# Kernel optimization log

Measured on AMD Instinct MI355X. Metric: run time of the kernel, lower is better.

## Reference

```python
import jax, jax.numpy as jnp
import numpy as np
import math

B, T = 64, 2000
RNN_DIM, EMB_DIM, ATT_DIM = 1024, 512, 128
STATIC_CH, STATIC_K = 8, 21
DYN_CH, DYN_K = 8, 21
PRIOR_LEN, ALPHA, BETA = 11, 0.1, 0.9


def _betabinom_pmf(k, n, a, b):
    lg = math.lgamma
    return math.exp(lg(n + 1) - lg(k + 1) - lg(n - k + 1)
                    + lg(k + a) + lg(n - k + b) - lg(n + a + b)
                    - (lg(a) + lg(b) - lg(a + b)))


def setup_inputs() -> dict:
    key = jax.random.key(0)
    ks = jax.random.split(key, 12)
    query = jax.random.normal(ks[0], (B, RNN_DIM), jnp.float32)
    memory = jax.random.normal(ks[1], (B, T, EMB_DIM), jnp.float32)
    a = jax.random.uniform(ks[2], (B, T), jnp.float32)
    alignment_pre = a / jnp.sum(a, axis=1, keepdims=True)  # valid attention distribution
    mask = jnp.zeros((B, T), dtype=bool)
    s = 1.0 / math.sqrt(RNN_DIM)
    W_w = jax.random.uniform(ks[3], (ATT_DIM, RNN_DIM), jnp.float32, -s, s)
    W_b = jax.random.uniform(ks[4], (ATT_DIM,), jnp.float32, -s, s)
    V_w = jax.random.normal(ks[5], (DYN_CH * DYN_K, ATT_DIM), jnp.float32) * 0.05
    F_w = jax.random.normal(ks[6], (STATIC_CH, 1, STATIC_K), jnp.float32) * 0.1
    U_w = jax.random.normal(ks[7], (ATT_DIM, STATIC_CH), jnp.float32) * 0.1
    T_w = jax.random.normal(ks[8], (ATT_DIM, DYN_CH), jnp.float32) * 0.1
    T_b = jax.random.normal(ks[9], (ATT_DIM,), jnp.float32) * 0.05
    v_w = jax.random.normal(ks[10], (1, ATT_DIM), jnp.float32) * 0.1
    P_np = np.array([_betabinom_pmf(k, PRIOR_LEN - 1, ALPHA, BETA) for k in range(PRIOR_LEN)], np.float32)
    P = jnp.asarray(P_np[::-1].copy())  # buffer: flipped beta-binomial prior
    return {"attention_hidden_state": query, "memory": memory, "alignment_pre": alignment_pre,
            "mask": mask, "W_w": W_w, "W_b": W_b, "V_w": V_w, "F_w": F_w,
            "U_w": U_w, "T_w": T_w, "T_b": T_b, "v_w": v_w, "P": P}


def _conv1d(lhs, rhs, pad, groups=1):
    # lhs [N,C,T], rhs [O,C//groups,K]; cross-correlation, matching torch conv1d
    return jax.lax.conv_general_dilated(lhs, rhs, (1,), [pad],
                                        dimension_numbers=("NCH", "OIH", "NCH"),
                                        feature_group_count=groups)


def reference(attention_hidden_state, memory, alignment_pre, mask,
              W_w, W_b, V_w, F_w, U_w, T_w, T_b, v_w, P):
    b, t = alignment_pre.shape
    # log of causal beta-binomial prior: left-pad by prior_length-1, valid conv
    p = _conv1d(alignment_pre[:, None, :], P.reshape(1, 1, -1), (PRIOR_LEN - 1, 0))[:, 0, :]
    p = jnp.log(jnp.clip(p, 1e-6))
    # per-sample dynamic kernels: [B, dyn_ch*K]
    G = jnp.tanh(attention_hidden_state @ W_w.T + W_b) @ V_w.T
    g = _conv1d(alignment_pre[None, :, :], G.reshape(b * DYN_CH, 1, DYN_K),
                ((DYN_K - 1) // 2, (DYN_K - 1) // 2), groups=b)  # [1, B*dyn_ch, T]
    g = g.reshape(b, DYN_CH, t).transpose(0, 2, 1)  # [B, T, dyn_ch]
    # static conv features
    f = _conv1d(alignment_pre[:, None, :], F_w,
                ((STATIC_K - 1) // 2, (STATIC_K - 1) // 2)).transpose(0, 2, 1)  # [B, T, static_ch]
    e = (jnp.tanh(f @ U_w.T + g @ T_w.T + T_b) @ v_w.T)[..., 0] + p  # [B, T]
    e = jnp.where(mask, -jnp.inf, e)
    attention_weights = jax.nn.softmax(e, axis=1)
    attention_context = jnp.einsum("bt,bte->be", attention_weights, memory)
    return attention_context, attention_weights
```

## Files before the change

### kernel.cpp

```cpp
#include <hip/hip_runtime.h>

#define B_   64
#define T_   2000
#define RNN_ 1024
#define EMB_ 512
#define ATT_ 128
#define CH_  8
#define K_   21
#define PL_  11
#define GSZ  168
#define ECHK 128
#define NEC  16
#define NCS  16
#define CPS  32
#define WSEG 125

typedef float vf4 __attribute__((ext_vector_type(4)));

__device__ __forceinline__ float fast_tanh(float x) {
    float ax = fabsf(x);
    float e  = __expf(2.0f * ax);
    float t  = 1.0f - 2.0f / (e + 1.0f);
    return copysignf(t, x);
}

__global__ __launch_bounds__(256) void k_gen_dyn(
    const float* __restrict__ q, const float* __restrict__ Ww,
    const float* __restrict__ Wb, const float* __restrict__ Vw,
    float* __restrict__ G)
{
    __shared__ float sq[RNN_];
    __shared__ float part[256];
    __shared__ float sh[ATT_];
    const int b = blockIdx.x, tid = threadIdx.x;
    for (int i = tid; i < RNN_; i += 256) sq[i] = q[b * RNN_ + i];
    __syncthreads();
    {
        const int row = tid & 127, half = tid >> 7;
        const float4* wr = reinterpret_cast<const float4*>(Ww + row * RNN_ + half * (RNN_ / 2));
        const float4* qr = reinterpret_cast<const float4*>(sq + half * (RNN_ / 2));
        float acc = 0.f;
        #pragma unroll 8
        for (int i = 0; i < RNN_ / 8; ++i) {
            float4 w4 = wr[i], q4 = qr[i];
            acc += w4.x * q4.x + w4.y * q4.y + w4.z * q4.z + w4.w * q4.w;
        }
        part[tid] = acc;
    }
    __syncthreads();
    if (tid < ATT_) sh[tid] = fast_tanh(part[tid] + part[tid + 128] + Wb[tid]);
    __syncthreads();
    for (int o = tid; o < GSZ; o += 256) {
        const float4* vr = reinterpret_cast<const float4*>(Vw + o * ATT_);
        const float4* hr = reinterpret_cast<const float4*>(sh);
        float acc = 0.f;
        #pragma unroll 8
        for (int i = 0; i < ATT_ / 4; ++i) {
            float4 v4 = vr[i], h4 = hr[i];
            acc += v4.x * h4.x + v4.y * h4.y + v4.z * h4.z + v4.w * h4.w;
        }
        G[b * GSZ + o] = acc;
    }
}

__global__ __launch_bounds__(256) void k_energy(
    const float* __restrict__ a,  const float* __restrict__ G,
    const float* __restrict__ Fw, const float* __restrict__ Uw,
    const float* __restrict__ Tw, const float* __restrict__ Tb,
    const float* __restrict__ vw, const float* __restrict__ P,
    const unsigned char* __restrict__ mask,
    float* __restrict__ pws, float* __restrict__ mred, float* __restrict__ sred)
{
    __shared__ float sA[ECHK + K_ - 1];
    __shared__ float sFG[K_ * 16];
    __shared__ float sUT[ATT_ * 16];
    __shared__ float sTb[ATT_], sV[ATT_], sPr[PL_];
    __shared__ float sQ[2 * ECHK];
    __shared__ float red[4];
    const int b = blockIdx.x, chunk = blockIdx.y, tid = threadIdx.x;
    const int t0 = chunk * ECHK;
    const int base = t0 - (K_ - 1) / 2;
    const int tloc = tid & (ECHK - 1);
    const int h = tid >> 7;

    for (int j = tid; j < ECHK + K_ - 1; j += 256) {
        int idx = base + j;
        sA[j] = (idx >= 0 && idx < T_) ? a[b * T_ + idx] : 0.f;
    }
    for (int j = tid; j < 2 * GSZ; j += 256) {
        if (j < GSZ) sFG[(j % K_) * 16 + (j / K_)] = Fw[j];
        else { int jj = j - GSZ; sFG[(jj % K_) * 16 + 8 + (jj / K_)] = G[b * GSZ + jj]; }
    }
    for (int j = tid; j < ATT_ * CH_; j += 256) {
        int d = j >> 3, c = j & 7;
        sUT[d * 16 + c]     = Uw[j];
        sUT[d * 16 + 8 + c] = Tw[j];
    }
    if (tid < ATT_) { sTb[tid] = Tb[tid]; sV[tid] = vw[tid]; }
    if (tid < PL_)  sPr[tid] = P[tid];
    __syncthreads();

    float fg[16];
    #pragma unroll
    for (int i = 0; i < 16; ++i) fg[i] = 0.f;
    #pragma unroll
    for (int k = 0; k < K_; ++k) {
        float av = sA[tloc + k];
        const float4* fp = reinterpret_cast<const float4*>(&sFG[k * 16]);
        float4 x0 = fp[0], x1 = fp[1], x2 = fp[2], x3 = fp[3];
        fg[0]  += x0.x * av; fg[1]  += x0.y * av; fg[2]  += x0.z * av; fg[3]  += x0.w * av;
        fg[4]  += x1.x * av; fg[5]  += x1.y * av; fg[6]  += x1.z * av; fg[7]  += x1.w * av;
        fg[8]  += x2.x * av; fg[9]  += x2.y * av; fg[10] += x2.z * av; fg[11] += x2.w * av;
        fg[12] += x3.x * av; fg[13] += x3.y * av; fg[14] += x3.z * av; fg[15] += x3.w * av;
    }

    float accQ = 0.f;
    const int d0 = h * 64;
    #pragma unroll 4
    for (int dd = 0; dd < 64; ++dd) {
        const int d = d0 + dd;
        const float4* up = reinterpret_cast<const float4*>(&sUT[d * 16]);
        float4 u0 = up[0], u1 = up[1], u2 = up[2], u3 = up[3];
        float s0 = u0.x * fg[0]  + u0.y * fg[1]  + u0.z * fg[2]  + u0.w * fg[3];
        float s1 = u1.x * fg[4]  + u1.y * fg[5]  + u1.z * fg[6]  + u1.w * fg[7];
        float s2 = u2.x * fg[8]  + u2.y * fg[9]  + u2.z * fg[10] + u2.w * fg[11];
        float s3 = u3.x * fg[12] + u3.y * fg[13] + u3.z * fg[14] + u3.w * fg[15];
        float s = (sTb[d] + s0) + (s1 + s2) + s3;
        accQ += sV[d] * fast_tanh(s);
    }
    sQ[h * ECHK + tloc] = accQ;
    __syncthreads();

    float e = -1e30f;
    const int t = t0 + tid;
    if (tid < ECHK) {
        const bool valid = (t < T_) && !mask[b * T_ + min(t, T_ - 1)];
        if (valid) {
            float pp = 0.f;
            #pragma unroll
            for (int k = 0; k < PL_; ++k) pp += sPr[k] * sA[tid + k];
            e = sQ[tid] + sQ[ECHK + tid] + __logf(fmaxf(pp, 1e-6f));
        }
    }
    float m = e;
    #pragma unroll
    for (int off = 32; off > 0; off >>= 1) m = fmaxf(m, __shfl_xor(m, off));
    if ((tid & 63) == 0) red[tid >> 6] = m;
    __syncthreads();
    const float Mc = fmaxf(fmaxf(red[0], red[1]), fmaxf(red[2], red[3]));
    __syncthreads();
    float pv = (e > -1e29f) ? __expf(e - Mc) : 0.f;
    if (tid < ECHK && t < T_) pws[b * T_ + t] = pv;
    float ssum = pv;
    #pragma unroll
    for (int off = 32; off > 0; off >>= 1) ssum += __shfl_xor(ssum, off);
    if ((tid & 63) == 0) red[tid >> 6] = ssum;
    __syncthreads();
    if (tid == 0) {
        mred[b * NEC + chunk] = Mc;
        sred[b * NEC + chunk] = red[0] + red[1] + red[2] + red[3];
    }
}

__global__ __launch_bounds__(256) void k_ctx(
    const float* __restrict__ mred, const float* __restrict__ sred,
    const float* __restrict__ pws, const float* __restrict__ mem,
    float* __restrict__ wout, float* __restrict__ out)
{
    __shared__ float sAl[NEC];
    __shared__ float sw_[T_];
    __shared__ vf4 sPart[32][8];
    const int b = blockIdx.x, cs = blockIdx.y, tid = threadIdx.x;

    if (tid < NEC) {
        float M = -1e30f;
        #pragma unroll
        for (int i = 0; i < NEC; ++i) M = fmaxf(M, mred[b * NEC + i]);
        float S = 0.f;
        #pragma unroll
        for (int i = 0; i < NEC; ++i) S += sred[b * NEC + i] * __expf(mred[b * NEC + i] - M);
        sAl[tid] = __expf(mred[b * NEC + tid] - M) / S;
    }
    __syncthreads();
    for (int j = tid; j < T_; j += 256) sw_[j] = pws[b * T_ + j] * sAl[j >> 7];
    __syncthreads();
    if (tid < WSEG) {
        const int t = cs * WSEG + tid;
        wout[b * T_ + t] = sw_[t];
    }

    const int lane = tid & 7, rgrp = tid >> 3;
    const float* basep = mem + (size_t)b * T_ * EMB_ + cs * CPS + lane * 4;
    vf4 acc = {0.f, 0.f, 0.f, 0.f};
    #pragma unroll 8
    for (int i = 0; i < 62; ++i) {
        const int t = rgrp + i * 32;
        vf4 mv = *reinterpret_cast<const vf4*>(basep + (size_t)t * EMB_);
        acc += sw_[t] * mv;
    }
    if (rgrp < 16) {
        const int t = rgrp + 1984;
        vf4 mv = *reinterpret_cast<const vf4*>(basep + (size_t)t * EMB_);
        acc += sw_[t] * mv;
    }
    sPart[rgrp][lane] = acc;
    __syncthreads();
    if (tid < 64) {
        const int l = tid & 7, qg = tid >> 3;
        vf4 r = sPart[qg][l] + sPart[qg + 8][l] + sPart[qg + 16][l] + sPart[qg + 24][l];
        sPart[qg][l] = r;
    }
    __syncthreads();
    if (tid < 8) {
        vf4 r = sPart[0][tid] + sPart[1][tid] + sPart[2][tid] + sPart[3][tid]
              + sPart[4][tid] + sPart[5][tid] + sPart[6][tid] + sPart[7][tid];
        *reinterpret_cast<vf4*>(out + b * EMB_ + cs * CPS + tid * 4) = r;
    }
}

extern "C" void kernel_launch(void* const* d_in, const int* in_sizes, int n_in,
                              void* d_out, int out_size, void* d_ws, size_t ws_size,
                              hipStream_t stream)
{
    const float* q    = (const float*)d_in[0];
    const float* mem  = (const float*)d_in[1];
    const float* a    = (const float*)d_in[2];
    const unsigned char* mask = (const unsigned char*)d_in[3];
    const float* Ww = (const float*)d_in[4];
    const float* Wb = (const float*)d_in[5];
    const float* Vw = (const float*)d_in[6];
    const float* Fw = (const float*)d_in[7];
    const float* Uw = (const float*)d_in[8];
    const float* Tw = (const float*)d_in[9];
    const float* Tb = (const float*)d_in[10];
    const float* vw = (const float*)d_in[11];
    const float* P  = (const float*)d_in[12];

    float* out_ctx = (float*)d_out;
    float* out_w   = out_ctx + B_ * EMB_;

    float* G    = (float*)d_ws;
    float* mred = G + B_ * GSZ;
    float* sred = mred + B_ * NEC;
    float* pws  = sred + B_ * NEC;

    k_gen_dyn<<<B_, 256, 0, stream>>>(q, Ww, Wb, Vw, G);
    k_energy<<<dim3(B_, NEC), 256, 0, stream>>>(a, G, Fw, Uw, Tw, Tb, vw, P,
                                                mask, pws, mred, sred);
    k_ctx<<<dim3(B_, NCS), 256, 0, stream>>>(mred, sred, pws, mem, out_w, out_ctx);
}
```

Before: 97.60 us.

## Fuse all three stages into one persistent kernel with per-batch grid barriers

Replaces the three kernel launches with a single 16x64-block kernel. The 16 blocks of each batch row cooperate through spin-wait barriers on global counters, first computing the hidden projection and the dynamic filters in split form, then energies for 125-step chunks. Each block then weights its own memory rows and atomically adds the partial context, which removes the pws round-trip and the launch gaps. The cost is a memset per call, spin-barrier latency, atomic contention on the output, and a deadlock risk if not all 1024 blocks can be resident at once.

After: 312.9 us. +220.6%, slower.

```diff
diff --git a/kernel.cpp b/kernel.cpp
--- a/kernel.cpp
+++ b/kernel.cpp
@@ -1,19 +1,16 @@
 #include <hip/hip_runtime.h>
 
-#define B_   64
-#define T_   2000
-#define RNN_ 1024
-#define EMB_ 512
-#define ATT_ 128
-#define CH_  8
-#define K_   21
-#define PL_  11
-#define GSZ  168
-#define ECHK 128
-#define NEC  16
-#define NCS  16
-#define CPS  32
-#define WSEG 125
+#define B_    64
+#define T_    2000
+#define RNN_  1024
+#define EMB_  512
+#define ATT_  128
+#define CH_   8
+#define K_    21
+#define PL_   11
+#define GSZ   168
+#define NC    16
+#define CROWS 125
 
 typedef float vf4 __attribute__((ext_vector_type(4)));
 
@@ -24,197 +21,224 @@
     return copysignf(t, x);
 }
 
-__global__ __launch_bounds__(256) void k_gen_dyn(
-    const float* __restrict__ q, const float* __restrict__ Ww,
-    const float* __restrict__ Wb, const float* __restrict__ Vw,
-    float* __restrict__ G)
+__device__ __forceinline__ void batch_bar(unsigned* bar, int slot, int b) {
+    __syncthreads();
+    if (threadIdx.x == 0) {
+        __threadfence();
+        unsigned* p = bar + slot * 64 + b;
+        atomicAdd(p, 1u);
+        long long tries = 0;
+        while (atomicAdd(p, 0u) < 16u) {
+            __builtin_amdgcn_s_sleep(2);
+            if (++tries > 200000000ll) break;
+        }
+        __threadfence();
+    }
+    __syncthreads();
+}
+
+__global__ __launch_bounds__(256, 4) void k_all(
+    const float* __restrict__ q,   const float* __restrict__ mem,
+    const float* __restrict__ a,   const unsigned char* __restrict__ mask,
+    const float* __restrict__ Ww,  const float* __restrict__ Wb,
+    const float* __restrict__ Vw,  const float* __restrict__ Fw,
+    const float* __restrict__ Uw,  const float* __restrict__ Tw,
+    const float* __restrict__ Tb,  const float* __restrict__ vw,
+    const float* __restrict__ P,
+    unsigned* __restrict__ bar,    float* __restrict__ h_ws,
+    float* __restrict__ G_ws,      float* __restrict__ mred,
+    float* __restrict__ sred,
+    float* __restrict__ out_ctx,   float* __restrict__ out_w)
 {
-    __shared__ float sq[RNN_];
-    __shared__ float part[256];
-    __shared__ float sh[ATT_];
-    const int b = blockIdx.x, tid = threadIdx.x;
-    for (int i = tid; i < RNN_; i += 256) sq[i] = q[b * RNN_ + i];
-    __syncthreads();
-    {
-        const int row = tid & 127, half = tid >> 7;
-        const float4* wr = reinterpret_cast<const float4*>(Ww + row * RNN_ + half * (RNN_ / 2));
-        const float4* qr = reinterpret_cast<const float4*>(sq + half * (RNN_ / 2));
+    __shared__ union {
+        struct { float q[RNN_]; float part[8][33]; } A;
+        struct { float h[ATT_]; float part[16][17]; } A2;
+        struct { float win[160]; float FG[K_ * 16]; float UT[ATT_ * 16];
+                 float Tb[ATT_]; float V[ATT_]; float Pr[12]; float Q[256];
+                 float red[4]; } B;
+        struct { float ms[32]; vf4 part[2][128]; } C;
+    } sm;
+    __shared__ float sp[128];
+
+    const int c = blockIdx.x, b = blockIdx.y, tid = threadIdx.x;
+    const int t0 = c * CROWS;
+
+    if (c == 0) {
+        for (int i = tid; i < EMB_; i += 256) out_ctx[b * EMB_ + i] = 0.f;
+    }
+    for (int i = tid; i < RNN_ / 4; i += 256)
+        reinterpret_cast<vf4*>(sm.A.q)[i] =
+            reinterpret_cast<const vf4*>(q + b * RNN_)[i];
+    __syncthreads();
+    {
+        const int dl = tid >> 5, ks = tid & 31;
+        const int d  = c * 8 + dl;
+        const vf4* wr = reinterpret_cast<const vf4*>(Ww + d * RNN_ + ks * 32);
+        const vf4* qr = reinterpret_cast<const vf4*>(sm.A.q + ks * 32);
         float acc = 0.f;
-        #pragma unroll 8
-        for (int i = 0; i < RNN_ / 8; ++i) {
-            float4 w4 = wr[i], q4 = qr[i];
+        #pragma unroll
+        for (int i = 0; i < 8; ++i) {
+            vf4 w4 = wr[i], q4 = qr[i];
             acc += w4.x * q4.x + w4.y * q4.y + w4.z * q4.z + w4.w * q4.w;
         }
-        part[tid] = acc;
-    }
-    __syncthreads();
-    if (tid < ATT_) sh[tid] = fast_tanh(part[tid] + part[tid + 128] + Wb[tid]);
-    __syncthreads();
-    for (int o = tid; o < GSZ; o += 256) {
-        const float4* vr = reinterpret_cast<const float4*>(Vw + o * ATT_);
-        const float4* hr = reinterpret_cast<const float4*>(sh);
+        sm.A.part[dl][ks] = acc;
+    }
+    __syncthreads();
+    if (tid < 8) {
+        float s = 0.f;
+        #pragma unroll
+        for (int i = 0; i < 32; ++i) s += sm.A.part[tid][i];
+        const int d = c * 8 + tid;
+        h_ws[b * ATT_ + d] = fast_tanh(s + Wb[d]);
+    }
+    batch_bar(bar, 0, b);
+
+    if (tid < ATT_) sm.A2.h[tid] = h_ws[b * ATT_ + tid];
+    __syncthreads();
+    {
+        const int j = tid >> 4, ks = tid & 15;
+        const int o = c * 11 + j;
         float acc = 0.f;
-        #pragma unroll 8
-        for (int i = 0; i < ATT_ / 4; ++i) {
-            float4 v4 = vr[i], h4 = hr[i];
-            acc += v4.x * h4.x + v4.y * h4.y + v4.z * h4.z + v4.w * h4.w;
-        }
-        G[b * GSZ + o] = acc;
-    }
-}
-
-__global__ __launch_bounds__(256) void k_energy(
-    const float* __restrict__ a,  const float* __restrict__ G,
-    const float* __restrict__ Fw, const float* __restrict__ Uw,
-    const float* __restrict__ Tw, const float* __restrict__ Tb,
-    const float* __restrict__ vw, const float* __restrict__ P,
-    const unsigned char* __restrict__ mask,
-    float* __restrict__ pws, float* __restrict__ mred, float* __restrict__ sred)
-{
-    __shared__ float sA[ECHK + K_ - 1];
-    __shared__ float sFG[K_ * 16];
-    __shared__ float sUT[ATT_ * 16];
-    __shared__ float sTb[ATT_], sV[ATT_], sPr[PL_];
-    __shared__ float sQ[2 * ECHK];
-    __shared__ float red[4];
-    const int b = blockIdx.x, chunk = blockIdx.y, tid = threadIdx.x;
-    const int t0 = chunk * ECHK;
-    const int base = t0 - (K_ - 1) / 2;
-    const int tloc = tid & (ECHK - 1);
-    const int h = tid >> 7;
-
-    for (int j = tid; j < ECHK + K_ - 1; j += 256) {
-        int idx = base + j;
-        sA[j] = (idx >= 0 && idx < T_) ? a[b * T_ + idx] : 0.f;
+        if (j < 11 && o < GSZ) {
+            const vf4* vr = reinterpret_cast<const vf4*>(Vw + o * ATT_ + ks * 8);
+            const vf4* hr = reinterpret_cast<const vf4*>(sm.A2.h + ks * 8);
+            vf4 v0 = vr[0], h0 = hr[0], v1 = vr[1], h1 = hr[1];
+            acc = v0.x * h0.x + v0.y * h0.y + v0.z * h0.z + v0.w * h0.w
+                + v1.x * h1.x + v1.y * h1.y + v1.z * h1.z + v1.w * h1.w;
+        }
+        sm.A2.part[j][ks] = acc;
+    }
+    __syncthreads();
+    if (tid < 11) {
+        const int o = c * 11 + tid;
+        if (o < GSZ) {
+            float s = 0.f;
+            #pragma unroll
+            for (int i = 0; i < 16; ++i) s += sm.A2.part[tid][i];
+            G_ws[b * GSZ + o] = s;
+        }
+    }
+    batch_bar(bar, 1, b);
+
+    for (int j = tid; j < CROWS + K_ - 1; j += 256) {
+        int idx = t0 - 10 + j;
+        sm.B.win[j] = (idx >= 0 && idx < T_) ? a[b * T_ + idx] : 0.f;
     }
     for (int j = tid; j < 2 * GSZ; j += 256) {
-        if (j < GSZ) sFG[(j % K_) * 16 + (j / K_)] = Fw[j];
-        else { int jj = j - GSZ; sFG[(jj % K_) * 16 + 8 + (jj / K_)] = G[b * GSZ + jj]; }
+        if (j < GSZ) sm.B.FG[(j % K_) * 16 + (j / K_)] = Fw[j];
+        else { int jj = j - GSZ; sm.B.FG[(jj % K_) * 16 + 8 + (jj / K_)] = G_ws[b * GSZ + jj]; }
     }
     for (int j = tid; j < ATT_ * CH_; j += 256) {
-        int d = j >> 3, c = j & 7;
-        sUT[d * 16 + c]     = Uw[j];
-        sUT[d * 16 + 8 + c] = Tw[j];
-    }
-    if (tid < ATT_) { sTb[tid] = Tb[tid]; sV[tid] = vw[tid]; }
-    if (tid < PL_)  sPr[tid] = P[tid];
-    __syncthreads();
-
-    float fg[16];
-    #pragma unroll
-    for (int i = 0; i < 16; ++i) fg[i] = 0.f;
-    #pragma unroll
-    for (int k = 0; k < K_; ++k) {
-        float av = sA[tloc + k];
-        const float4* fp = reinterpret_cast<const float4*>(&sFG[k * 16]);
-        float4 x0 = fp[0], x1 = fp[1], x2 = fp[2], x3 = fp[3];
-        fg[0]  += x0.x * av; fg[1]  += x0.y * av; fg[2]  += x0.z * av; fg[3]  += x0.w * av;
-        fg[4]  += x1.x * av; fg[5]  += x1.y * av; fg[6]  += x1.z * av; fg[7]  += x1.w * av;
-        fg[8]  += x2.x * av; fg[9]  += x2.y * av; fg[10] += x2.z * av; fg[11] += x2.w * av;
-        fg[12] += x3.x * av; fg[13] += x3.y * av; fg[14] += x3.z * av; fg[15] += x3.w * av;
-    }
-
-    float accQ = 0.f;
-    const int d0 = h * 64;
-    #pragma unroll 4
-    for (int dd = 0; dd < 64; ++dd) {
-        const int d = d0 + dd;
-        const float4* up = reinterpret_cast<const float4*>(&sUT[d * 16]);
-        float4 u0 = up[0], u1 = up[1], u2 = up[2], u3 = up[3];
-        float s0 = u0.x * fg[0]  + u0.y * fg[1]  + u0.z * fg[2]  + u0.w * fg[3];
-        float s1 = u1.x * fg[4]  + u1.y * fg[5]  + u1.z * fg[6]  + u1.w * fg[7];
-        float s2 = u2.x * fg[8]  + u2.y * fg[9]  + u2.z * fg[10] + u2.w * fg[11];
-        float s3 = u3.x * fg[12] + u3.y * fg[13] + u3.z * fg[14] + u3.w * fg[15];
-        float s = (sTb[d] + s0) + (s1 + s2) + s3;
-        accQ += sV[d] * fast_tanh(s);
-    }
-    sQ[h * ECHK + tloc] = accQ;
+        int d = j >> 3, ch = j & 7;
+        sm.B.UT[d * 16 + ch]     = Uw[j];
+        sm.B.UT[d * 16 + 8 + ch] = Tw[j];
+    }
+    if (tid < ATT_) { sm.B.Tb[tid] = Tb[tid]; sm.B.V[tid] = vw[tid]; }
+    if (tid < PL_)  sm.B.Pr[tid] = P[tid];
+    __syncthreads();
+
+    const int tloc = tid & 127, half = tid >> 7;
+    {
+        float fg[16];
+        #pragma unroll
+        for (int i = 0; i < 16; ++i) fg[i] = 0.f;
+        #pragma unroll
+        for (int k = 0; k < K_; ++k) {
+            float av = sm.B.win[tloc + k];
+            const vf4* fp = reinterpret_cast<const vf4*>(&sm.B.FG[k * 16]);
+            vf4 x0 = fp[0], x1 = fp[1], x2 = fp[2], x3 = fp[3];
+            fg[0]  += x0.x * av; fg[1]  += x0.y * av; fg[2]  += x0.z * av; fg[3]  += x0.w * av;
+            fg[4]  += x1.x * av; fg[5]  += x1.y * av; fg[6]  += x1.z * av; fg[7]  += x1.w * av;
+            fg[8]  += x2.x * av; fg[9]  += x2.y * av; fg[10] += x2.z * av; fg[11] += x2.w * av;
+            fg[12] += x3.x * av; fg[13] += x3.y * av; fg[14] += x3.z * av; fg[15] += x3.w * av;
+        }
+        float accQ = 0.f;
+        const int d0 = half * 64;
+        #pragma unroll 4
+        for (int dd = 0; dd < 64; ++dd) {
+            const int d = d0 + dd;
+            const vf4* up = reinterpret_cast<const vf4*>(&sm.B.UT[d * 16]);
+            vf4 u0 = up[0], u1 = up[1], u2 = up[2], u3 = up[3];
+            float s0 = u0.x * fg[0]  + u0.y * fg[1]  + u0.z * fg[2]  + u0.w * fg[3];
+            float s1 = u1.x * fg[4]  + u1.y * fg[5]  + u1.z * fg[6]  + u1.w * fg[7];
+            float s2 = u2.x * fg[8]  + u2.y * fg[9]  + u2.z * fg[10] + u2.w * fg[11];
+            float s3 = u3.x * fg[12] + u3.y * fg[13] + u3.z * fg[14] + u3.w * fg[15];
+            float s = (sm.B.Tb[d] + s0) + (s1 + s2) + s3;
+            accQ += sm.B.V[d] * fast_tanh(s);
+        }
+        sm.B.Q[half * 128 + tloc] = accQ;
+    }
     __syncthreads();
 
     float e = -1e30f;
-    const int t = t0 + tid;
-    if (tid < ECHK) {
-        const bool valid = (t < T_) && !mask[b * T_ + min(t, T_ - 1)];
-        if (valid) {
+    if (tid < CROWS) {
+        const int t = t0 + tid;
+        if (!mask[b * T_ + t]) {
             float pp = 0.f;
             #pragma unroll
-            for (int k = 0; k < PL_; ++k) pp += sPr[k] * sA[tid + k];
-            e = sQ[tid] + sQ[ECHK + tid] + __logf(fmaxf(pp, 1e-6f));
+            for (int k = 0; k < PL_; ++k) pp += sm.B.Pr[k] * sm.B.win[tid + k];
+            e = sm.B.Q[tid] + sm.B.Q[128 + tid] + __logf(fmaxf(pp, 1e-6f));
         }
     }
     float m = e;
     #pragma unroll
     for (int off = 32; off > 0; off >>= 1) m = fmaxf(m, __shfl_xor(m, off));
-    if ((tid & 63) == 0) red[tid >> 6] = m;
-    __syncthreads();
-    const float Mc = fmaxf(fmaxf(red[0], red[1]), fmaxf(red[2], red[3]));
+    if ((tid & 63) == 0) sm.B.red[tid >> 6] = m;
+    __syncthreads();
+    const float Mc = fmaxf(fmaxf(sm.B.red[0], sm.B.red[1]),
+                           fmaxf(sm.B.red[2], sm.B.red[3]));
     __syncthreads();
     float pv = (e > -1e29f) ? __expf(e - Mc) : 0.f;
-    if (tid < ECHK && t < T_) pws[b * T_ + t] = pv;
+    if (tid < 128) sp[tid] = (tid < CROWS) ? pv : 0.f;
     float ssum = pv;
     #pragma unroll
     for (int off = 32; off > 0; off >>= 1) ssum += __shfl_xor(ssum, off);
-    if ((tid & 63) == 0) red[tid >> 6] = ssum;
+    if ((tid & 63) == 0) sm.B.red[tid >> 6] = ssum;
     __syncthreads();
     if (tid == 0) {
-        mred[b * NEC + chunk] = Mc;
-        sred[b * NEC + chunk] = red[0] + red[1] + red[2] + red[3];
-    }
-}
-
-__global__ __launch_bounds__(256) void k_ctx(
-    const float* __restrict__ mred, const float* __restrict__ sred,
-    const float* __restrict__ pws, const float* __restrict__ mem,
-    float* __restrict__ wout, float* __restrict__ out)
-{
-    __shared__ float sAl[NEC];
-    __shared__ float sw_[T_];
-    __shared__ vf4 sPart[32][8];
-    const int b = blockIdx.x, cs = blockIdx.y, tid = threadIdx.x;
-
-    if (tid < NEC) {
-        float M = -1e30f;
-        #pragma unroll
-        for (int i = 0; i < NEC; ++i) M = fmaxf(M, mred[b * NEC + i]);
-        float S = 0.f;
-        #pragma unroll
-        for (int i = 0; i < NEC; ++i) S += sred[b * NEC + i] * __expf(mred[b * NEC + i] - M);
-        sAl[tid] = __expf(mred[b * NEC + tid] - M) / S;
-    }
-    __syncthreads();
-    for (int j = tid; j < T_; j += 256) sw_[j] = pws[b * T_ + j] * sAl[j >> 7];
-    __syncthreads();
-    if (tid < WSEG) {
-        const int t = cs * WSEG + tid;
-        wout[b * T_ + t] = sw_[t];
-    }
-
-    const int lane = tid & 7, rgrp = tid >> 3;
-    const float* basep = mem + (size_t)b * T_ * EMB_ + cs * CPS + lane * 4;
-    vf4 acc = {0.f, 0.f, 0.f, 0.f};
-    #pragma unroll 8
-    for (int i = 0; i < 62; ++i) {
-        const int t = rgrp + i * 32;
-        vf4 mv = *reinterpret_cast<const vf4*>(basep + (size_t)t * EMB_);
-        acc += sw_[t] * mv;
-    }
-    if (rgrp < 16) {
-        const int t = rgrp + 1984;
-        vf4 mv = *reinterpret_cast<const vf4*>(basep + (size_t)t * EMB_);
-        acc += sw_[t] * mv;
-    }
-    sPart[rgrp][lane] = acc;
-    __syncthreads();
-    if (tid < 64) {
-        const int l = tid & 7, qg = tid >> 3;
-        vf4 r = sPart[qg][l] + sPart[qg + 8][l] + sPart[qg + 16][l] + sPart[qg + 24][l];
-        sPart[qg][l] = r;
-    }
-    __syncthreads();
-    if (tid < 8) {
-        vf4 r = sPart[0][tid] + sPart[1][tid] + sPart[2][tid] + sPart[3][tid]
-              + sPart[4][tid] + sPart[5][tid] + sPart[6][tid] + sPart[7][tid];
-        *reinterpret_cast<vf4*>(out + b * EMB_ + cs * CPS + tid * 4) = r;
+        mred[b * NC + c] = Mc;
+        sred[b * NC + c] = sm.B.red[0] + sm.B.red[1] + sm.B.red[2] + sm.B.red[3];
+    }
+    batch_bar(bar, 2, b);
+
+    if (tid < NC) {
+        sm.C.ms[tid]      = mred[b * NC + tid];
+        sm.C.ms[16 + tid] = sred[b * NC + tid];
+    }
+    __syncthreads();
+    float M = sm.C.ms[0];
+    #pragma unroll
+    for (int i = 1; i < NC; ++i) M = fmaxf(M, sm.C.ms[i]);
+    float S = 0.f;
+    #pragma unroll
+    for (int i = 0; i < NC; ++i) S += sm.C.ms[16 + i] * __expf(sm.C.ms[i] - M);
+    const float alpha = __expf(sm.C.ms[c] - M) / S;
+    __syncthreads();
+    if (tid < CROWS) {
+        float wv = sp[tid] * alpha;
+        sp[tid] = wv;
+        out_w[b * T_ + t0 + tid] = wv;
+    }
+    __syncthreads();
+
+    {
+        const int col = tid & 127, rp = tid >> 7;
+        const float* basep = mem + ((size_t)(b * T_ + t0)) * EMB_ + col * 4;
+        vf4 acc = {0.f, 0.f, 0.f, 0.f};
+        #pragma unroll 8
+        for (int r = rp; r < CROWS; r += 2) {
+            vf4 mv = *reinterpret_cast<const vf4*>(basep + (size_t)r * EMB_);
+            acc += sp[r] * mv;
+        }
+        sm.C.part[rp][col] = acc;
+    }
+    __syncthreads();
+    if (tid < 128) {
+        vf4 r = sm.C.part[0][tid];
+        r += sm.C.part[1][tid];
+        float* op = out_ctx + b * EMB_ + tid * 4;
+        atomicAdd(op + 0, r.x); atomicAdd(op + 1, r.y);
+        atomicAdd(op + 2, r.z); atomicAdd(op + 3, r.w);
     }
 }
 
@@ -239,13 +263,15 @@
     float* out_ctx = (float*)d_out;
     float* out_w   = out_ctx + B_ * EMB_;
 
-    float* G    = (float*)d_ws;
-    float* mred = G + B_ * GSZ;
-    float* sred = mred + B_ * NEC;
-    float* pws  = sred + B_ * NEC;
-
-    k_gen_dyn<<<B_, 256, 0, stream>>>(q, Ww, Wb, Vw, G);
-    k_energy<<<dim3(B_, NEC), 256, 0, stream>>>(a, G, Fw, Uw, Tw, Tb, vw, P,
-                                                mask, pws, mred, sred);
-    k_ctx<<<dim3(B_, NCS), 256, 0, stream>>>(mred, sred, pws, mem, out_w, out_ctx);
-}
+    unsigned* bar = (unsigned*)d_ws;
+    float* h_ws = (float*)d_ws + 192;
+    float* G_ws = h_ws + B_ * ATT_;
+    float* mred = G_ws + B_ * GSZ;
+    float* sred = mred + B_ * NC;
+
+    hipMemsetAsync(bar, 0, 3 * 64 * sizeof(unsigned), stream);
+    k_all<<<dim3(NC, B_), 256, 0, stream>>>(q, mem, a, mask, Ww, Wb, Vw, Fw,
+                                            Uw, Tw, Tb, vw, P,
+                                            bar, h_ws, G_ws, mred, sred,
+                                            out_ctx, out_w);
+}
```
